# Optimization experiments

Hardware: AMD Instinct MI355X
Metric: run time of the kernel (lower is better)

The kernel has to match this reference:

```python
import jax, jax.numpy as jnp
import numpy as np

VOCAB, EMBED, FILT, LABELS = 30522, 256, 256, 50
B, S = 32, 4096

def setup_inputs() -> dict:
    key = jax.random.key(0)
    k0, k1, k2, k3, k4 = jax.random.split(key, 5)
    return {
        "input_ids": jax.random.randint(k0, (B, S), 0, VOCAB),
        "emb_table": jax.random.normal(k1, (VOCAB, EMBED), dtype=jnp.float32) * 0.02,
        "conv_w": jax.random.normal(k2, (FILT, EMBED, 4), dtype=jnp.float32) * 0.05,  # (out_ch, in_ch, k)
        "conv_b": jnp.zeros((FILT,), dtype=jnp.float32),
        "U_w": jax.random.normal(k3, (LABELS, FILT), dtype=jnp.float32) * 0.05,  # torch Linear weight layout
        "final_w": jax.random.normal(k4, (LABELS, FILT), dtype=jnp.float32) * 0.05,
        "final_b": jnp.zeros((LABELS,), dtype=jnp.float32),
    }

def reference(input_ids, emb_table, conv_w, conv_b, U_w, final_w, final_b):
    # Embedding lookup: (B, S, E) -> NCH layout (B, E, S)
    x = jnp.take(emb_table, input_ids, axis=0).transpose(0, 2, 1)
    # Conv1d(kernel=4, padding=2): output length S+1
    h = jax.lax.conv_general_dilated(
        x, conv_w, window_strides=(1,), padding=[(2, 2)],
        dimension_numbers=("NCH", "OIH", "NCH"))
    H = jnp.tanh(h + conv_b[None, :, None]).transpose(0, 2, 1)  # (B, S+1, F)
    # Per-label attention: softmax over the sequence dimension
    scores = jnp.einsum("bsf,lf->bsl", H, U_w)          # (B, S+1, L)
    alpha = jax.nn.softmax(scores, axis=1)
    m = jnp.einsum("bsl,bsf->blf", alpha, H)             # (B, L, F)
    logits = jnp.sum(m * final_w[None], axis=2) + final_b  # (B, L)
    return logits
```

## Files before the change

### kernel.cpp

```cpp
#include <hip/hip_runtime.h>
#include <hip/hip_bf16.h>
#include <stdint.h>

#define BDIM 32
#define SDIM 4096
#define SP1  4097
#define EDIM 256
#define FDIM 256
#define LDIM 50
#define TTILE 128
#define NT    32

typedef __attribute__((ext_vector_type(8))) short bf16x8v;
typedef __attribute__((ext_vector_type(4))) float f32x4;

__device__ __forceinline__ unsigned short f2bf(float f) {
    union { float f; uint32_t u; } v; v.f = f;
    uint32_t u = v.u;
    uint32_t r = (u + 0x7fffu + ((u >> 16) & 1u)) >> 16;
    return (unsigned short)r;
}

__device__ __forceinline__ float bf2f(unsigned short s) {
    union { uint32_t u; float f; } v; v.u = (uint32_t)s << 16; return v.f;
}

__device__ __forceinline__ float tanh_fast(float x) {
    float e = __expf(2.0f * x);
    float r = __builtin_amdgcn_rcpf(e + 1.0f);
    return fmaf(-2.0f, r, 1.0f);
}

__device__ __forceinline__ uint32_t pack_bf2(float lo, float hi) {
    union { __hip_bfloat162 v; uint32_t u; } cv;
    cv.v = __halves2bfloat162(__float2bfloat16(lo), __float2bfloat16(hi));
    return cv.u;
}

__device__ __forceinline__ void load_lds16(const void* g, uint32_t* l) {
    __builtin_amdgcn_global_load_lds(
        (const __attribute__((address_space(1))) uint32_t*)g,
        (__attribute__((address_space(3))) uint32_t*)l, 16, 0, 0);
}

__global__ void prep_all(const float* __restrict__ emb, const float* __restrict__ conv_w,
                         const float* __restrict__ U_w, const float* __restrict__ final_w,
                         unsigned short* __restrict__ embb, unsigned short* __restrict__ Wb2,
                         unsigned short* __restrict__ W2k, uint32_t* __restrict__ zp)
{
    int o = blockIdx.x * 256 + threadIdx.x;
    size_t eo = (size_t)o * 8;
    if (eo < (size_t)30522 * 256) {
        float4 v0 = *(const float4*)(emb + eo);
        float4 v1 = *(const float4*)(emb + eo + 4);
        union { unsigned short u[8]; uint4 q; } pk;
        pk.u[0] = f2bf(v0.x); pk.u[1] = f2bf(v0.y); pk.u[2] = f2bf(v0.z); pk.u[3] = f2bf(v0.w);
        pk.u[4] = f2bf(v1.x); pk.u[5] = f2bf(v1.y); pk.u[6] = f2bf(v1.z); pk.u[7] = f2bf(v1.w);
        *(uint4*)(embb + eo) = pk.q;
    }
    if (o < 262144) {
        int kk = o & 1023, f = o >> 10;
        int e = kk & 255, k = kk >> 8;
        int g = kk >> 5, h4 = (kk >> 3) & 3, j = kk & 7;
        Wb2[((size_t)(g * 4 + h4) * 256 + f) * 8 + j] = f2bf(conv_w[f * 1024 + e * 4 + k]);
    }
    if (o < 32768) {
        int j = o & 7, c = (o >> 3) & 127, g = o >> 10;
        int k = g * 8 + j, l = c & 63;
        float v = 0.f;
        if (l < LDIM) v = (c < 64) ? U_w[l * FDIM + k] : final_w[l * FDIM + k];
        W2k[o] = f2bf(v);
    }
    if (o < 128) zp[o] = 0;
}

__global__ __launch_bounds__(256, 2) void fused_kernel(
    const int* __restrict__ ids, const unsigned short* __restrict__ embb,
    const unsigned short* __restrict__ Wb2, const float* __restrict__ conv_b,
    const unsigned short* __restrict__ W2k, const uint32_t* __restrict__ zp,
    const float* __restrict__ U_w, const float* __restrict__ final_w,
    float* __restrict__ part)
{
    __shared__ uint32_t xs[133 * 128];

    const int tid  = threadIdx.x;
    const int lane = tid & 63;
    const int wid  = tid >> 6;
    const int b    = blockIdx.y;
    const int tile = blockIdx.x;
    const int t0   = tile * TTILE;
    const int l15  = lane & 15;
    const int hi4  = lane >> 4;
    const int q    = lane & 31;
    const int half = lane >> 5;

    {
        int nid[17];
        #pragma unroll
        for (int j = 0; j < 17; ++j) {
            int r0 = wid * 2 + j * 8;
            int r  = r0 + half;
            int p  = t0 - 2 + r;
            nid[j] = -1;
            if (r0 < 131 && r < 131 && (unsigned)p < SDIM)
                nid[j] = ids[b * SDIM + p];
        }
        const unsigned short* zs = (const unsigned short*)zp + q * 8;
        #pragma unroll
        for (int j = 0; j < 17; ++j) {
            int r0 = wid * 2 + j * 8;
            if (r0 >= 131) continue;
            int r = r0 + half;
            const unsigned short* s = (nid[j] >= 0)
                ? embb + (size_t)nid[j] * EDIM + (((uint32_t)(q * 16) ^ ((uint32_t)(r & 7) << 4)) >> 1)
                : zs;
            load_lds16(s, &xs[r0 * 128]);
        }
    }
    __syncthreads();

    const int fbase = wid * 64;
    const unsigned short* afbase = Wb2 + (size_t)(hi4 * 256 + fbase + l15) * 8;

    f32x4 acc[4][8];
    #pragma unroll
    for (int a = 0; a < 4; ++a)
        #pragma unroll
        for (int n = 0; n < 8; ++n) acc[a][n] = (f32x4){0.f, 0.f, 0.f, 0.f};

    bf16x8v afc[4];
    #pragma unroll
    for (int a = 0; a < 4; ++a) afc[a] = *(const bf16x8v*)(afbase + a * 128);

    #pragma unroll 1
    for (int k = 0; k < 4; ++k) {
        uint32_t bb[8];
        #pragma unroll
        for (int n = 0; n < 8; ++n) {
            int r = n * 16 + l15 + k;
            bb[n] = (uint32_t)(r * 512) ^ (uint32_t)(hi4 * 16) ^ (uint32_t)((r & 7) << 4);
        }
        const unsigned short* afg = afbase + (size_t)k * 65536;
        #pragma unroll
        for (int es = 0; es < 8; ++es) {
            const unsigned short* nxt = (es < 7)
                ? (afg + (size_t)(es + 1) * 8192)
                : (afbase + (size_t)((k + 1) & 3) * 65536);
            bf16x8v afn[4];
            #pragma unroll
            for (int a = 0; a < 4; ++a) afn[a] = *(const bf16x8v*)(nxt + a * 128);

            bf16x8v bfr[8];
            #pragma unroll
            for (int n = 0; n < 8; ++n)
                bfr[n] = *(const bf16x8v*)((const char*)xs + (bb[n] ^ (uint32_t)(es * 64)));

            __builtin_amdgcn_s_setprio(1);
            #pragma unroll
            for (int a = 0; a < 4; ++a)
                #pragma unroll
                for (int n = 0; n < 8; ++n)
                    acc[a][n] = __builtin_amdgcn_mfma_f32_16x16x32_bf16(afc[a], bfr[n], acc[a][n], 0, 0, 0);
            __builtin_amdgcn_s_setprio(0);

            #pragma unroll
            for (int a = 0; a < 4; ++a) afc[a] = afn[a];
        }
    }
    __syncthreads();

    float4 cb[4];
    #pragma unroll
    for (int a = 0; a < 4; ++a)
        cb[a] = *(const float4*)(conv_b + fbase + a * 16 + hi4 * 4);
    #pragma unroll
    for (int n = 0; n < 8; ++n) {
        int tl = n * 16 + l15;
        uint32_t hb = (uint32_t)(tl * 512) ^ (uint32_t)(hi4 * 8)
                    ^ (uint32_t)(fbase * 2) ^ (uint32_t)((tl & 7) << 4);
        #pragma unroll
        for (int a = 0; a < 4; ++a) {
            f32x4 d = acc[a][n];
            uint2 pk;
            pk.x = pack_bf2(tanh_fast(d[0] + cb[a].x), tanh_fast(d[1] + cb[a].y));
            pk.y = pack_bf2(tanh_fast(d[2] + cb[a].z), tanh_fast(d[3] + cb[a].w));
            *(uint2*)((char*)xs + (hb ^ (uint32_t)(a * 32))) = pk;
        }
    }
    __syncthreads();

    const int cbase = wid * 16;
    f32x4 p2[8][2];
    #pragma unroll
    for (int m = 0; m < 8; ++m) { p2[m][0] = (f32x4){0,0,0,0}; p2[m][1] = (f32x4){0,0,0,0}; }

    uint32_t pb[8];
    #pragma unroll
    for (int m = 0; m < 8; ++m) {
        int sl = m * 16 + l15;
        pb[m] = (uint32_t)(sl * 512) ^ (uint32_t)(hi4 * 16) ^ (uint32_t)((sl & 7) << 4);
    }
    const unsigned short* wp0 = W2k + (size_t)(hi4 * 128 + cbase + l15) * 8;

    #pragma unroll
    for (int step = 0; step < 8; ++step) {
        bf16x8v ha[8], w2[2];
        #pragma unroll
        for (int m = 0; m < 8; ++m)
            ha[m] = *(const bf16x8v*)((const char*)xs + (pb[m] ^ (uint32_t)(step * 64)));
        w2[0] = *(const bf16x8v*)(wp0 + step * 4096);
        w2[1] = *(const bf16x8v*)(wp0 + 512 + step * 4096);
        __builtin_amdgcn_s_setprio(1);
        #pragma unroll
        for (int m = 0; m < 8; ++m) {
            p2[m][0] = __builtin_amdgcn_mfma_f32_16x16x32_bf16(ha[m], w2[0], p2[m][0], 0, 0, 0);
            p2[m][1] = __builtin_amdgcn_mfma_f32_16x16x32_bf16(ha[m], w2[1], p2[m][1], 0, 0, 0);
        }
        __builtin_amdgcn_s_setprio(0);
    }

    float mx = -1e30f;
    #pragma unroll
    for (int m = 0; m < 8; ++m)
        #pragma unroll
        for (int i = 0; i < 4; ++i)
            mx = fmaxf(mx, p2[m][0][i]);
    float se = 0.f, st = 0.f;
    #pragma unroll
    for (int m = 0; m < 8; ++m)
        #pragma unroll
        for (int i = 0; i < 4; ++i) {
            float e = __expf(p2[m][0][i] - mx);
            se += e;
            st += e * p2[m][1][i];
        }
    #pragma unroll
    for (int d = 16; d <= 32; d <<= 1) {
        float mo  = __shfl_xor(mx, d);
        float seo = __shfl_xor(se, d);
        float sto = __shfl_xor(st, d);
        float M  = fmaxf(mx, mo);
        float w0 = __expf(mx - M), w1 = __expf(mo - M);
        se = se * w0 + seo * w1;
        st = st * w0 + sto * w1;
        mx = M;
    }
    if (lane < 16) {
        int l = cbase + l15;
        if (l < LDIM) {
            size_t o = (((size_t)b * (NT + 1) + tile) * LDIM + l) * 3;
            part[o] = mx; part[o + 1] = se; part[o + 2] = st;
        }
    }

    if (tile == NT - 1) {
        __syncthreads();
        float* hs4 = (float*)xs;
        float* rsc = hs4 + 256;
        float* rtv = hs4 + 512;
        const int f = tid;

        float a0 = 0.f, a1 = 0.f;
        #pragma unroll 2
        for (int tap = 0; tap < 2; ++tap) {
            int r = 128 + tap;
            uint32_t swz = (uint32_t)((r & 7) << 4);
            #pragma unroll
            for (int es = 0; es < 8; ++es) {
                #pragma unroll
                for (int h4 = 0; h4 < 4; ++h4) {
                    int g = tap * 8 + es;
                    bf16x8v w = *(const bf16x8v*)(Wb2 + ((size_t)(g * 4 + h4) * 256 + f) * 8);
                    int e0 = es * 32 + h4 * 8;
                    uint32_t byte = (uint32_t)(r * 512) + ((uint32_t)(e0 * 2) ^ swz);
                    const unsigned short* xv = (const unsigned short*)((const char*)xs + byte);
                    float s = 0.f;
                    #pragma unroll
                    for (int j = 0; j < 8; ++j)
                        s = fmaf(bf2f((unsigned short)w[j]), bf2f(xv[j]), s);
                    if (tap == 0) a0 += s; else a1 += s;
                }
            }
        }
        float hv = tanh_fast(conv_b[f] + a0 + a1);
        __syncthreads();
        hs4[f] = hv;
        __syncthreads();

        {
            const int l = tid & 63, c = tid >> 6;
            float sc = 0.f, tv = 0.f;
            if (l < LDIM) {
                const float4* uw = (const float4*)(U_w + (size_t)l * FDIM + c * 64);
                const float4* fw = (const float4*)(final_w + (size_t)l * FDIM + c * 64);
                const float4* hh = (const float4*)(hs4 + c * 64);
                #pragma unroll
                for (int i = 0; i < 16; ++i) {
                    float4 h = hh[i], u = uw[i], w = fw[i];
                    sc = fmaf(h.x, u.x, fmaf(h.y, u.y, fmaf(h.z, u.z, fmaf(h.w, u.w, sc))));
                    tv = fmaf(h.x, w.x, fmaf(h.y, w.y, fmaf(h.z, w.z, fmaf(h.w, w.w, tv))));
                }
            }
            rsc[tid] = sc; rtv[tid] = tv;
        }
        __syncthreads();

        if (tid < LDIM) {
            float sc = rsc[tid] + rsc[tid + 64] + rsc[tid + 128] + rsc[tid + 192];
            float tv = rtv[tid] + rtv[tid + 64] + rtv[tid + 128] + rtv[tid + 192];
            size_t o = (((size_t)b * (NT + 1) + NT) * LDIM + tid) * 3;
            part[o] = sc; part[o + 1] = 1.0f; part[o + 2] = tv;
        }
    }
}

__global__ __launch_bounds__(64) void final_kernel(
    const float* __restrict__ part, const float* __restrict__ final_b,
    float* __restrict__ out)
{
    int b = blockIdx.x, l = threadIdx.x;
    if (l >= LDIM) return;
    float mx = -1e30f, se = 0.f, st = 0.f;
    for (int c = 0; c <= NT; ++c) {
        size_t o = (((size_t)b * (NT + 1) + c) * LDIM + l) * 3;
        float mo = part[o], seo = part[o + 1], sto = part[o + 2];
        float M  = fmaxf(mx, mo);
        float w0 = __expf(mx - M), w1 = __expf(mo - M);
        se = se * w0 + seo * w1;
        st = st * w0 + sto * w1;
        mx = M;
    }
    out[b * LDIM + l] = st / se + final_b[l];
}

extern "C" void kernel_launch(void* const* d_in, const int* in_sizes, int n_in,
                              void* d_out, int out_size, void* d_ws, size_t ws_size,
                              hipStream_t stream)
{
    const int*   ids     = (const int*)d_in[0];
    const float* emb     = (const float*)d_in[1];
    const float* conv_w  = (const float*)d_in[2];
    const float* conv_b  = (const float*)d_in[3];
    const float* U_w     = (const float*)d_in[4];
    const float* final_w = (const float*)d_in[5];
    const float* final_b = (const float*)d_in[6];

    char* ws = (char*)d_ws;
    size_t offE  = 0;
    size_t szE   = (size_t)30522 * 256 * 2;
    size_t offWb = offE + szE;
    size_t szWb  = 256 * 1024 * 2;
    size_t offW2 = offWb + szWb;
    size_t szW2  = 32768 * 2;
    size_t offZ  = offW2 + szW2;
    size_t szZ   = 512;
    size_t offP  = offZ + szZ;

    unsigned short* embb = (unsigned short*)(ws + offE);
    unsigned short* Wb2  = (unsigned short*)(ws + offWb);
    unsigned short* W2k  = (unsigned short*)(ws + offW2);
    uint32_t*       zp   = (uint32_t*)(ws + offZ);
    float*          prt  = (float*)(ws + offP);

    prep_all<<<3816, 256, 0, stream>>>(emb, conv_w, U_w, final_w, embb, Wb2, W2k, zp);
    fused_kernel<<<dim3(NT, BDIM), 256, 0, stream>>>(ids, embb, Wb2, conv_b, W2k, zp,
                                                     U_w, final_w, prt);
    final_kernel<<<BDIM, 64, 0, stream>>>(prt, final_b, (float*)d_out);
}
```

Before: 108.4 us.

## Move tail sequence-position computation out of fused kernel into prep kernel

The extra final output position (S+1 tail), which the last tile of each batch used to compute after its main work, now runs in 32 dedicated blocks of a new prep kernel alongside the embedding-to-bf16 conversion. The weight-packing prep is split into its own small kernel that runs first, since the tail computation needs the packed conv weights. This removes the serialized tail work from the last-tile blocks, which likely set the fused kernel's critical path, and shrinks its LDS allocation by one row. The cost is an extra kernel launch and one more dependency step before the main kernel.

```diff
diff --git a/kernel.cpp b/kernel.cpp
--- a/kernel.cpp
+++ b/kernel.cpp
@@ -43,22 +43,13 @@
         (__attribute__((address_space(3))) uint32_t*)l, 16, 0, 0);
 }
 
-__global__ void prep_all(const float* __restrict__ emb, const float* __restrict__ conv_w,
-                         const float* __restrict__ U_w, const float* __restrict__ final_w,
-                         unsigned short* __restrict__ embb, unsigned short* __restrict__ Wb2,
-                         unsigned short* __restrict__ W2k, uint32_t* __restrict__ zp)
+__global__ void prep_w(const float* __restrict__ conv_w,
+                       const float* __restrict__ U_w, const float* __restrict__ final_w,
+                       unsigned short* __restrict__ Wb2, unsigned short* __restrict__ W2k,
+                       uint32_t* __restrict__ zp)
 {
     int o = blockIdx.x * 256 + threadIdx.x;
-    size_t eo = (size_t)o * 8;
-    if (eo < (size_t)30522 * 256) {
-        float4 v0 = *(const float4*)(emb + eo);
-        float4 v1 = *(const float4*)(emb + eo + 4);
-        union { unsigned short u[8]; uint4 q; } pk;
-        pk.u[0] = f2bf(v0.x); pk.u[1] = f2bf(v0.y); pk.u[2] = f2bf(v0.z); pk.u[3] = f2bf(v0.w);
-        pk.u[4] = f2bf(v1.x); pk.u[5] = f2bf(v1.y); pk.u[6] = f2bf(v1.z); pk.u[7] = f2bf(v1.w);
-        *(uint4*)(embb + eo) = pk.q;
-    }
-    if (o < 262144) {
+    {
         int kk = o & 1023, f = o >> 10;
         int e = kk & 255, k = kk >> 8;
         int g = kk >> 5, h4 = (kk >> 3) & 3, j = kk & 7;
@@ -74,14 +65,89 @@
     if (o < 128) zp[o] = 0;
 }
 
+__global__ __launch_bounds__(256) void prep_emb_special(
+    const float* __restrict__ emb, const int* __restrict__ ids,
+    const unsigned short* __restrict__ Wb2, const float* __restrict__ conv_b,
+    const float* __restrict__ U_w, const float* __restrict__ final_w,
+    unsigned short* __restrict__ embb, float* __restrict__ part)
+{
+    __shared__ float x0[256], x1[256], hsh[256], rsc[256], rtv[256];
+    const int tid = threadIdx.x;
+    const int idx = blockIdx.x;
+
+    if (idx < BDIM) {
+        const int b = idx;
+        const int f = tid;
+        {
+            int id0 = ids[b * SDIM + 4094];
+            int id1 = ids[b * SDIM + 4095];
+            x0[f] = emb[(size_t)id0 * EDIM + f];
+            x1[f] = emb[(size_t)id1 * EDIM + f];
+        }
+        __syncthreads();
+
+        float a0 = 0.f, a1 = 0.f;
+        #pragma unroll
+        for (int g = 0; g < 16; ++g) {
+            const float* xv = (g < 8) ? x0 : x1;
+            #pragma unroll
+            for (int h4 = 0; h4 < 4; ++h4) {
+                bf16x8v w = *(const bf16x8v*)(Wb2 + ((size_t)(g * 4 + h4) * 256 + f) * 8);
+                int e0 = (g & 7) * 32 + h4 * 8;
+                float s = 0.f;
+                #pragma unroll
+                for (int j = 0; j < 8; ++j)
+                    s = fmaf(bf2f((unsigned short)w[j]), xv[e0 + j], s);
+                if (g < 8) a0 += s; else a1 += s;
+            }
+        }
+        hsh[f] = tanh_fast(conv_b[f] + a0 + a1);
+        __syncthreads();
+
+        {
+            const int l = tid & 63, c = tid >> 6;
+            float sc = 0.f, tv = 0.f;
+            if (l < LDIM) {
+                const float4* uw = (const float4*)(U_w + (size_t)l * FDIM + c * 64);
+                const float4* fw = (const float4*)(final_w + (size_t)l * FDIM + c * 64);
+                const float4* hh = (const float4*)(hsh + c * 64);
+                #pragma unroll
+                for (int i = 0; i < 16; ++i) {
+                    float4 h = hh[i], u = uw[i], w = fw[i];
+                    sc = fmaf(h.x, u.x, fmaf(h.y, u.y, fmaf(h.z, u.z, fmaf(h.w, u.w, sc))));
+                    tv = fmaf(h.x, w.x, fmaf(h.y, w.y, fmaf(h.z, w.z, fmaf(h.w, w.w, tv))));
+                }
+            }
+            rsc[tid] = sc; rtv[tid] = tv;
+        }
+        __syncthreads();
+
+        if (tid < LDIM) {
+            float sc = rsc[tid] + rsc[tid + 64] + rsc[tid + 128] + rsc[tid + 192];
+            float tv = rtv[tid] + rtv[tid + 64] + rtv[tid + 128] + rtv[tid + 192];
+            size_t o = (((size_t)b * (NT + 1) + NT) * LDIM + tid) * 3;
+            part[o] = sc; part[o + 1] = 1.0f; part[o + 2] = tv;
+        }
+    } else {
+        size_t o = ((size_t)(idx - BDIM) * 256 + tid) * 8;
+        if (o < (size_t)30522 * 256) {
+            float4 v0 = *(const float4*)(emb + o);
+            float4 v1 = *(const float4*)(emb + o + 4);
+            union { unsigned short u[8]; uint4 q; } pk;
+            pk.u[0] = f2bf(v0.x); pk.u[1] = f2bf(v0.y); pk.u[2] = f2bf(v0.z); pk.u[3] = f2bf(v0.w);
+            pk.u[4] = f2bf(v1.x); pk.u[5] = f2bf(v1.y); pk.u[6] = f2bf(v1.z); pk.u[7] = f2bf(v1.w);
+            *(uint4*)(embb + o) = pk.q;
+        }
+    }
+}
+
 __global__ __launch_bounds__(256, 2) void fused_kernel(
     const int* __restrict__ ids, const unsigned short* __restrict__ embb,
     const unsigned short* __restrict__ Wb2, const float* __restrict__ conv_b,
     const unsigned short* __restrict__ W2k, const uint32_t* __restrict__ zp,
-    const float* __restrict__ U_w, const float* __restrict__ final_w,
     float* __restrict__ part)
 {
-    __shared__ uint32_t xs[133 * 128];
+    __shared__ uint32_t xs[132 * 128];
 
     const int tid  = threadIdx.x;
     const int lane = tid & 63;
@@ -250,66 +316,6 @@
         if (l < LDIM) {
             size_t o = (((size_t)b * (NT + 1) + tile) * LDIM + l) * 3;
             part[o] = mx; part[o + 1] = se; part[o + 2] = st;
-        }
-    }
-
-    if (tile == NT - 1) {
-        __syncthreads();
-        float* hs4 = (float*)xs;
-        float* rsc = hs4 + 256;
-        float* rtv = hs4 + 512;
-        const int f = tid;
-
-        float a0 = 0.f, a1 = 0.f;
-        #pragma unroll 2
-        for (int tap = 0; tap < 2; ++tap) {
-            int r = 128 + tap;
-            uint32_t swz = (uint32_t)((r & 7) << 4);
-            #pragma unroll
-            for (int es = 0; es < 8; ++es) {
-                #pragma unroll
-                for (int h4 = 0; h4 < 4; ++h4) {
-                    int g = tap * 8 + es;
-                    bf16x8v w = *(const bf16x8v*)(Wb2 + ((size_t)(g * 4 + h4) * 256 + f) * 8);
-                    int e0 = es * 32 + h4 * 8;
-                    uint32_t byte = (uint32_t)(r * 512) + ((uint32_t)(e0 * 2) ^ swz);
-                    const unsigned short* xv = (const unsigned short*)((const char*)xs + byte);
-                    float s = 0.f;
-                    #pragma unroll
-                    for (int j = 0; j < 8; ++j)
-                        s = fmaf(bf2f((unsigned short)w[j]), bf2f(xv[j]), s);
-                    if (tap == 0) a0 += s; else a1 += s;
-                }
-            }
-        }
-        float hv = tanh_fast(conv_b[f] + a0 + a1);
-        __syncthreads();
-        hs4[f] = hv;
-        __syncthreads();
-
-        {
-            const int l = tid & 63, c = tid >> 6;
-            float sc = 0.f, tv = 0.f;
-            if (l < LDIM) {
-                const float4* uw = (const float4*)(U_w + (size_t)l * FDIM + c * 64);
-                const float4* fw = (const float4*)(final_w + (size_t)l * FDIM + c * 64);
-                const float4* hh = (const float4*)(hs4 + c * 64);
-                #pragma unroll
-                for (int i = 0; i < 16; ++i) {
-                    float4 h = hh[i], u = uw[i], w = fw[i];
-                    sc = fmaf(h.x, u.x, fmaf(h.y, u.y, fmaf(h.z, u.z, fmaf(h.w, u.w, sc))));
-                    tv = fmaf(h.x, w.x, fmaf(h.y, w.y, fmaf(h.z, w.z, fmaf(h.w, w.w, tv))));
-                }
-            }
-            rsc[tid] = sc; rtv[tid] = tv;
-        }
-        __syncthreads();
-
-        if (tid < LDIM) {
-            float sc = rsc[tid] + rsc[tid + 64] + rsc[tid + 128] + rsc[tid + 192];
-            float tv = rtv[tid] + rtv[tid + 64] + rtv[tid + 128] + rtv[tid + 192];
-            size_t o = (((size_t)b * (NT + 1) + NT) * LDIM + tid) * 3;
-            part[o] = sc; part[o + 1] = 1.0f; part[o + 2] = tv;
         }
     }
 }
@@ -362,8 +368,9 @@
     uint32_t*       zp   = (uint32_t*)(ws + offZ);
     float*          prt  = (float*)(ws + offP);
 
-    prep_all<<<3816, 256, 0, stream>>>(emb, conv_w, U_w, final_w, embb, Wb2, W2k, zp);
-    fused_kernel<<<dim3(NT, BDIM), 256, 0, stream>>>(ids, embb, Wb2, conv_b, W2k, zp,
-                                                     U_w, final_w, prt);
+    prep_w<<<1024, 256, 0, stream>>>(conv_w, U_w, final_w, Wb2, W2k, zp);
+    prep_emb_special<<<3816 + BDIM, 256, 0, stream>>>(emb, ids, Wb2, conv_b,
+                                                      U_w, final_w, embb, prt);
+    fused_kernel<<<dim3(NT, BDIM), 256, 0, stream>>>(ids, embb, Wb2, conv_b, W2k, zp, prt);
     final_kernel<<<BDIM, 64, 0, stream>>>(prt, final_b, (float*)d_out);
 }
```

Result: faster. 91.92 us, median of 2 (-15.2%).
